# Kernel optimization log

Hardware: AMD Instinct MI355X
Metric: run time of the kernel (lower is better)

The kernel has to match this reference:

```python
import jax, jax.numpy as jnp
import numpy as np

B, P, F = 8, 8192, 32          # clouds, points per cloud, feature dim
RATIO, R, K = 0.25, 0.2, 64    # fps ratio, ball radius, max neighbors
M = int(P * RATIO)             # centroids per cloud


def setup_inputs() -> dict:
    key = jax.random.key(0)
    ks = jax.random.split(key, 6)
    pos = jax.random.uniform(ks[0], (B * P, 3), dtype=jnp.float32)
    batch = jnp.repeat(jnp.arange(B, dtype=jnp.int32), P)
    x = jax.random.normal(ks[1], (B * P, F), dtype=jnp.float32)

    def lin(k, i, o):
        return jax.random.normal(k, (i, o), dtype=jnp.float32) * (1.0 / np.sqrt(i))

    return {
        "pos": pos, "batch": batch, "x": x,
        "W1": lin(ks[2], F + 3, 64), "b1": jnp.zeros((64,), jnp.float32),
        "W2": lin(ks[3], 64, 64),    "b2": jnp.zeros((64,), jnp.float32),
        "W3": lin(ks[4], 64, 128),   "b3": jnp.zeros((128,), jnp.float32),
    }


def _fps(pos_b):
    """Farthest point sampling on one cloud [P,3] -> [M] indices (start at 0)."""
    d0 = jnp.full((P,), jnp.inf, pos_b.dtype)

    def step(carry, _):
        dists, last = carry
        d = jnp.sum((pos_b - pos_b[last]) ** 2, axis=-1)
        dists = jnp.minimum(dists, d)
        nxt = jnp.argmax(dists).astype(jnp.int32)
        return (dists, nxt), nxt

    _, idx = jax.lax.scan(step, (d0, jnp.int32(0)), None, length=M - 1)
    return jnp.concatenate([jnp.zeros((1,), jnp.int32), idx])


def reference(pos, batch, x, W1, b1, W2, b2, W3, b3):
    posb = pos.reshape(B, P, 3)
    xb = x.reshape(B, P, F)

    # --- FPS: pick M pivot points per cloud ---
    idx = jax.vmap(_fps)(posb)                                   # [B,M]
    cent = jnp.take_along_axis(posb, idx[..., None], axis=1)     # [B,M,3]

    # --- radius ball query: up to K neighbors within R (lowest indices first) ---
    d2 = jnp.sum((cent[:, :, None, :] - posb[:, None, :, :]) ** 2, axis=-1)  # [B,M,P]
    in_ball = d2 <= R * R
    nb = jnp.sort(jnp.where(in_ball, jnp.arange(P)[None, None, :], P), axis=-1)[..., :K]
    valid = nb < P                                               # [B,M,K]
    nb_safe = jnp.where(valid, nb, 0)

    # --- gather -> point_filter MLP -> masked max aggregation (PointNetConv) ---
    pos_j = jax.vmap(lambda p, i: p[i])(posb, nb_safe)           # [B,M,K,3]
    x_j = jax.vmap(lambda f, i: f[i])(xb, nb_safe)               # [B,M,K,F]
    msg = jnp.concatenate([x_j, pos_j - cent[:, :, None, :]], axis=-1)  # [B,M,K,F+3]
    h = jax.nn.relu(msg @ W1 + b1)
    h = jax.nn.relu(h @ W2 + b2)
    h = jax.nn.relu(h @ W3 + b3)                                 # [B,M,K,128]
    neg = jnp.finfo(h.dtype).min
    h = jnp.where(valid[..., None], h, neg)
    out = jnp.max(h, axis=2)  # every centroid is its own neighbor -> non-empty

    centr_batch = jnp.repeat(jnp.arange(B, dtype=batch.dtype), M)
    return cent.reshape(B * M, 3), out.reshape(B * M, 128), centr_batch
```

## Files before the change

kernel.cpp:

```cpp
#include <hip/hip_runtime.h>
#include <stdint.h>
#include <math.h>

constexpr int kB = 8;
constexpr int kP = 8192;
constexpr int kF = 32;
constexpr int kM = 2048;
constexpr int kK = 64;
constexpr int kH = 64;
constexpr int kO = 128;

typedef float v2f __attribute__((ext_vector_type(2)));

__device__ __forceinline__ float dist2(float ax, float ay, float az,
                                       float bx, float by, float bz) {
#pragma clang fp contract(off)
    float dx = ax - bx, dy = ay - by, dz = az - bz;
    return (dx * dx + dy * dy) + dz * dz;
}

template <int CTRL>
__device__ __forceinline__ void dpp_max_step(unsigned int& khi, unsigned int& klo) {
    unsigned int ohi = (unsigned int)__builtin_amdgcn_update_dpp(
        0, (int)khi, CTRL, 0xf, 0xf, true);
    unsigned int olo = (unsigned int)__builtin_amdgcn_update_dpp(
        0, (int)klo, CTRL, 0xf, 0xf, true);
    bool take = (ohi > khi) || (ohi == khi && olo > klo);
    khi = take ? ohi : khi;
    klo = take ? olo : klo;
}

__global__ void init_kernel(int* __restrict__ prog) {
    if (threadIdx.x < 128) prog[threadIdx.x] = 0;
}

union SharedU {
    struct {
        float sxp[kP], syp[kP], szp[kP];
        unsigned short widx[kM];
        unsigned long long part[2][4];
    } f;
    struct {
        float msg[kK][36];
        float h1[kK][kH];
        float h2[kK][kH];
        float red[2][kO];
        int   s_nb[kK];
        float s_cent[3];
        int   s_cnt;
    } c;
};

__global__ __launch_bounds__(256, 1) void mega_kernel(
    const float* __restrict__ pos, const float* __restrict__ x,
    const float* __restrict__ W1, const float* __restrict__ b1,
    const float* __restrict__ W2, const float* __restrict__ b2,
    const float* __restrict__ W3, const float* __restrict__ b3,
    unsigned int* __restrict__ stage, int* __restrict__ prog,
    float* __restrict__ cent_out, float* __restrict__ feat_out,
    float* __restrict__ batch_out) {
    __shared__ SharedU sh;

    const int tid = threadIdx.x;
    const int wave = tid >> 6, lane = tid & 63;

    if (blockIdx.x < (unsigned)kB) {
        const int b = blockIdx.x;
        const float* pb = pos + (size_t)b * kP * 3;

        v2f px2[16], py2[16], pz2[16], dd2[16];
#pragma unroll
        for (int q = 0; q < 32; ++q) {
            int i = tid + q * 256;
            float X = pb[i * 3 + 0];
            float Y = pb[i * 3 + 1];
            float Z = pb[i * 3 + 2];
            sh.f.sxp[i] = X; sh.f.syp[i] = Y; sh.f.szp[i] = Z;
            if (q & 1) { px2[q >> 1].y = X; py2[q >> 1].y = Y; pz2[q >> 1].y = Z; }
            else       { px2[q >> 1].x = X; py2[q >> 1].x = Y; pz2[q >> 1].x = Z; }
        }
#pragma unroll
        for (int q = 0; q < 16; ++q) dd2[q] = (v2f){INFINITY, INFINITY};

        if (tid == 0) sh.f.widx[0] = 0;
        __syncthreads();

        float lx = sh.f.sxp[0], ly = sh.f.syp[0], lz = sh.f.szp[0];
        if (tid == 0) {
            size_t o = (size_t)(b * kM) * 3;
            __hip_atomic_store(&stage[o + 0], __float_as_uint(lx),
                               __ATOMIC_RELAXED, __HIP_MEMORY_SCOPE_AGENT);
            __hip_atomic_store(&stage[o + 1], __float_as_uint(ly),
                               __ATOMIC_RELAXED, __HIP_MEMORY_SCOPE_AGENT);
            __hip_atomic_store(&stage[o + 2], __float_as_uint(lz),
                               __ATOMIC_RELAXED, __HIP_MEMORY_SCOPE_AGENT);
            __hip_atomic_store(&prog[b * 16], 1,
                               __ATOMIC_RELEASE, __HIP_MEMORY_SCOPE_AGENT);
        }

        for (int m = 1; m < kM; ++m) {
            v2f lxv = {lx, lx}, lyv = {ly, ly}, lzv = {lz, lz};
#pragma unroll
            for (int q = 0; q < 16; ++q) {
#pragma clang fp contract(off)
                v2f dx = px2[q] - lxv;
                v2f dy = py2[q] - lyv;
                v2f dz = pz2[q] - lzv;
                v2f d2 = (dx * dx + dy * dy) + dz * dz;
                dd2[q].x = fminf(dd2[q].x, d2.x);
                dd2[q].y = fminf(dd2[q].y, d2.y);
            }

            v2f t0 = {fmaxf(dd2[0].x, dd2[0].y), fmaxf(dd2[1].x, dd2[1].y)};
            v2f t1 = {fmaxf(dd2[2].x, dd2[2].y), fmaxf(dd2[3].x, dd2[3].y)};
            v2f t2 = {fmaxf(dd2[4].x, dd2[4].y), fmaxf(dd2[5].x, dd2[5].y)};
            v2f t3 = {fmaxf(dd2[6].x, dd2[6].y), fmaxf(dd2[7].x, dd2[7].y)};
            v2f t4 = {fmaxf(dd2[8].x, dd2[8].y), fmaxf(dd2[9].x, dd2[9].y)};
            v2f t5 = {fmaxf(dd2[10].x, dd2[10].y), fmaxf(dd2[11].x, dd2[11].y)};
            v2f t6 = {fmaxf(dd2[12].x, dd2[12].y), fmaxf(dd2[13].x, dd2[13].y)};
            v2f t7 = {fmaxf(dd2[14].x, dd2[14].y), fmaxf(dd2[15].x, dd2[15].y)};
            float u0 = fmaxf(fmaxf(t0.x, t0.y), fmaxf(t1.x, t1.y));
            float u1 = fmaxf(fmaxf(t2.x, t2.y), fmaxf(t3.x, t3.y));
            float u2 = fmaxf(fmaxf(t4.x, t4.y), fmaxf(t5.x, t5.y));
            float u3 = fmaxf(fmaxf(t6.x, t6.y), fmaxf(t7.x, t7.y));
            float bv = fmaxf(fmaxf(u0, u1), fmaxf(u2, u3));

            int lqs[4];
#pragma unroll
            for (int g = 0; g < 4; ++g) {
                int t = 64;
#pragma unroll
                for (int s = 7; s >= 0; --s) {
                    int sl = g * 8 + s;
                    float v = (sl & 1) ? dd2[sl >> 1].y : dd2[sl >> 1].x;
                    t = (v == bv) ? sl : t;
                }
                lqs[g] = t;
            }
            int bq = lqs[3];
            bq = (lqs[2] < 64) ? lqs[2] : bq;
            bq = (lqs[1] < 64) ? lqs[1] : bq;
            bq = (lqs[0] < 64) ? lqs[0] : bq;

            unsigned int bidx = (unsigned int)(tid + bq * 256);
            unsigned int khi = __float_as_uint(bv);
            unsigned int klo = (unsigned int)(~bidx);

            dpp_max_step<0x111>(khi, klo);
            dpp_max_step<0x112>(khi, klo);
            dpp_max_step<0x114>(khi, klo);
            dpp_max_step<0x118>(khi, klo);
            dpp_max_step<0x142>(khi, klo);
            dpp_max_step<0x143>(khi, klo);
            if (lane == 63)
                sh.f.part[m & 1][wave] = ((unsigned long long)khi << 32) | klo;
            __syncthreads();

            unsigned long long k = sh.f.part[m & 1][0];
#pragma unroll
            for (int w = 1; w < 4; ++w) {
                unsigned long long o = sh.f.part[m & 1][w];
                if (o > k) k = o;
            }
            unsigned int wi = ~(unsigned int)k;
            lx = sh.f.sxp[wi]; ly = sh.f.syp[wi]; lz = sh.f.szp[wi];
            if (tid == 0) sh.f.widx[m] = (unsigned short)wi;

            if ((m & 31) == 31) {
                int m0 = m - 31;
                if (tid < 96) {
                    int mm = m0 + tid / 3;
                    int comp = tid % 3;
                    unsigned int w2 = (mm == m) ? wi
                                                : (unsigned int)sh.f.widx[mm];
                    float v = (comp == 0) ? sh.f.sxp[w2]
                            : (comp == 1) ? sh.f.syp[w2] : sh.f.szp[w2];
                    __hip_atomic_store(&stage[(size_t)(b * kM + mm) * 3 + comp],
                                       __float_as_uint(v),
                                       __ATOMIC_RELAXED, __HIP_MEMORY_SCOPE_AGENT);
                }
                __syncthreads();
                if (tid == 0)
                    __hip_atomic_store(&prog[b * 16], m + 1,
                                       __ATOMIC_RELEASE, __HIP_MEMORY_SCOPE_AGENT);
            }
        }
        __syncthreads();

#pragma unroll
        for (int q = 0; q < kM / 256; ++q) {
            int i = tid + q * 256;
            unsigned int wi = sh.f.widx[i];
            size_t o = (size_t)(b * kM + i) * 3;
            cent_out[o + 0] = sh.f.sxp[wi];
            cent_out[o + 1] = sh.f.syp[wi];
            cent_out[o + 2] = sh.f.szp[wi];
        }
        return;
    }

    const int i = (int)blockIdx.x - kB;
    const int b = i & 7;
    const int cl = i >> 3;
    const int c = b * kM + cl;

    if (tid == 0) {
        int p;
        while ((p = __hip_atomic_load(&prog[b * 16], __ATOMIC_ACQUIRE,
                                      __HIP_MEMORY_SCOPE_AGENT)) < cl + 1) {
            if (cl + 1 - p > 128) __builtin_amdgcn_s_sleep(64);
            else                  __builtin_amdgcn_s_sleep(8);
        }
    }
    __syncthreads();

    if (tid < 3) {
        unsigned int u = __hip_atomic_load(&stage[(size_t)c * 3 + tid],
                                           __ATOMIC_RELAXED, __HIP_MEMORY_SCOPE_AGENT);
        sh.c.s_cent[tid] = __uint_as_float(u);
    }
    __syncthreads();

    if (wave == 0) {
        const float R2 = (float)(0.2 * 0.2);
        float cx = sh.c.s_cent[0], cy = sh.c.s_cent[1], cz = sh.c.s_cent[2];
        const float* pb = pos + (size_t)b * kP * 3;
        int cnt = 0;
        for (int p0 = 0; p0 < kP && cnt < kK; p0 += 64) {
            int idx = p0 + lane;
            float X = pb[idx * 3 + 0], Y = pb[idx * 3 + 1], Z = pb[idx * 3 + 2];
            float d2 = dist2(X, Y, Z, cx, cy, cz);
            bool in = d2 <= R2;
            unsigned long long mask = __ballot(in);
            int rank = __popcll(mask & ((1ull << lane) - 1ull));
            if (in && cnt + rank < kK) sh.c.s_nb[cnt + rank] = idx;
            cnt = min(cnt + (int)__popcll(mask), kK);
        }
        if (lane == 0) { sh.c.s_cnt = cnt; batch_out[c] = (float)b; }
    }
    __syncthreads();
    const int cnt = sh.c.s_cnt;

    for (int u = tid; u < kK * 35; u += 256) {
        int k = u / 35, f = u - k * 35;
        float v = 0.0f;
        if (k < cnt) {
            int n = sh.c.s_nb[k];
            if (f < 32) v = x[((size_t)b * kP + n) * kF + f];
            else        v = pos[((size_t)b * kP + n) * 3 + (f - 32)] - sh.c.s_cent[f - 32];
        }
        sh.c.msg[k][f] = v;
    }
    __syncthreads();

    {
        int j = tid & 63, k0 = tid >> 6;
        float w[35];
#pragma unroll
        for (int q = 0; q < 35; ++q) w[q] = W1[q * 64 + j];
        float bb = b1[j];
#pragma unroll
        for (int kk = 0; kk < 16; ++kk) {
            int k = k0 * 16 + kk;
            float acc = bb;
#pragma unroll
            for (int q = 0; q < 35; ++q) acc += sh.c.msg[k][q] * w[q];
            sh.c.h1[k][j] = fmaxf(acc, 0.0f);
        }
    }
    __syncthreads();

    {
        int j = tid & 63, k0 = tid >> 6;
        float w[64];
#pragma unroll
        for (int q = 0; q < 64; ++q) w[q] = W2[q * 64 + j];
        float bb = b2[j];
#pragma unroll
        for (int kk = 0; kk < 16; ++kk) {
            int k = k0 * 16 + kk;
            float acc = bb;
#pragma unroll
            for (int q = 0; q < 64; ++q) acc += sh.c.h1[k][q] * w[q];
            sh.c.h2[k][j] = fmaxf(acc, 0.0f);
        }
    }
    __syncthreads();

    {
        int j = tid & 127, k0 = tid >> 7;
        float w[64];
#pragma unroll
        for (int q = 0; q < 64; ++q) w[q] = W3[q * 128 + j];
        float bb = b3[j];
        float best = -INFINITY;
        for (int kk = 0; kk < 32; ++kk) {
            int k = k0 * 32 + kk;
            if (k >= cnt) break;
            float acc = bb;
#pragma unroll
            for (int q = 0; q < 64; ++q) acc += sh.c.h2[k][q] * w[q];
            best = fmaxf(best, fmaxf(acc, 0.0f));
        }
        sh.c.red[k0][j] = best;
    }
    __syncthreads();

    if (tid < kO) {
        float o = fmaxf(sh.c.red[0][tid], sh.c.red[1][tid]);
        feat_out[(size_t)c * kO + tid] = o;
    }
}

extern "C" void kernel_launch(void* const* d_in, const int* in_sizes, int n_in,
                              void* d_out, int out_size, void* d_ws, size_t ws_size,
                              hipStream_t stream) {
    const float* pos = (const float*)d_in[0];
    const float* x  = (const float*)d_in[2];
    const float* W1 = (const float*)d_in[3];
    const float* b1 = (const float*)d_in[4];
    const float* W2 = (const float*)d_in[5];
    const float* b2 = (const float*)d_in[6];
    const float* W3 = (const float*)d_in[7];
    const float* b3 = (const float*)d_in[8];

    float* out = (float*)d_out;
    float* cent_out  = out;
    float* feat_out  = out + (size_t)kB * kM * 3;
    float* batch_out = out + (size_t)kB * kM * (3 + kO);

    char* ws = (char*)d_ws;
    int* prog           = (int*)ws;
    unsigned int* stage = (unsigned int*)(ws + 512);

    init_kernel<<<1, 128, 0, stream>>>(prog);
    mega_kernel<<<kB + kB * kM, 256, 0, stream>>>(
        pos, x, W1, b1, W2, b2, W3, b3, stage, prog,
        cent_out, feat_out, batch_out);
}
```

Before: 2.492 ms.

## Process four centroids per block and run the MLP on fp16 MFMA

Each consumer block now handles four centroids, one per wave. Each wave runs its own ball query and gathers its neighbors straight into fp16 shared tiles. The three MLP layers are rewritten as 16x16x32 f16 MFMA tiles against transposed fp16 weights staged once per block, with the masked max taken from the accumulators. This removes scalar FP32 FMA loops and cuts the block count fourfold, which spreads weight-loading cost across more work. The price is reduced fp16 precision for activations and weights, and each block must wait for four centroids from FPS before it starts.

```diff
diff --git a/kernel.cpp b/kernel.cpp
--- a/kernel.cpp
+++ b/kernel.cpp
@@ -7,10 +7,11 @@
 constexpr int kF = 32;
 constexpr int kM = 2048;
 constexpr int kK = 64;
-constexpr int kH = 64;
 constexpr int kO = 128;
 
 typedef float v2f __attribute__((ext_vector_type(2)));
+typedef _Float16 h8 __attribute__((ext_vector_type(8)));
+typedef float f4v __attribute__((ext_vector_type(4)));
 
 __device__ __forceinline__ float dist2(float ax, float ay, float az,
                                        float bx, float by, float bz) {
@@ -41,13 +42,15 @@
         unsigned long long part[2][4];
     } f;
     struct {
-        float msg[kK][36];
-        float h1[kK][kH];
-        float h2[kK][kH];
-        float red[2][kO];
-        int   s_nb[kK];
-        float s_cent[3];
-        int   s_cnt;
+        _Float16 A0[256][72];
+        _Float16 A1[256][72];
+        _Float16 Wt1[64][72];
+        _Float16 Wt2[64][72];
+        _Float16 Wt3[128][72];
+        float bias[256];
+        float red[4][4][128];
+        int   s_nb[4][kK];
+        int   s_cnt[4];
     } c;
 };
 
@@ -201,29 +204,39 @@
 
     const int i = (int)blockIdx.x - kB;
     const int b = i & 7;
-    const int cl = i >> 3;
-    const int c = b * kM + cl;
+    const int cl0 = (i >> 3) * 4;
+
+    for (int idx = tid; idx < 64 * 64; idx += 256) {
+        int n = idx & 63, kk = idx >> 6;
+        sh.c.Wt1[n][kk] = (_Float16)((kk < 35) ? W1[kk * 64 + n] : 0.0f);
+        sh.c.Wt2[n][kk] = (_Float16)W2[kk * 64 + n];
+    }
+    for (int idx = tid; idx < 64 * 128; idx += 256) {
+        int n = idx & 127, kk = idx >> 7;
+        sh.c.Wt3[n][kk] = (_Float16)W3[kk * 128 + n];
+    }
+    sh.c.bias[tid] = (tid < 64) ? b1[tid] : (tid < 128) ? b2[tid - 64]
+                                                        : b3[tid - 128];
 
     if (tid == 0) {
         int p;
         while ((p = __hip_atomic_load(&prog[b * 16], __ATOMIC_ACQUIRE,
-                                      __HIP_MEMORY_SCOPE_AGENT)) < cl + 1) {
-            if (cl + 1 - p > 128) __builtin_amdgcn_s_sleep(64);
-            else                  __builtin_amdgcn_s_sleep(8);
-        }
-    }
-    __syncthreads();
-
-    if (tid < 3) {
-        unsigned int u = __hip_atomic_load(&stage[(size_t)c * 3 + tid],
-                                           __ATOMIC_RELAXED, __HIP_MEMORY_SCOPE_AGENT);
-        sh.c.s_cent[tid] = __uint_as_float(u);
-    }
-    __syncthreads();
-
-    if (wave == 0) {
+                                      __HIP_MEMORY_SCOPE_AGENT)) < cl0 + 4) {
+            if (cl0 + 4 - p > 128) __builtin_amdgcn_s_sleep(64);
+            else                   __builtin_amdgcn_s_sleep(8);
+        }
+    }
+    __syncthreads();
+
+    const int c = b * kM + cl0 + wave;
+    float cx = __uint_as_float(__hip_atomic_load(&stage[(size_t)c * 3 + 0],
+                   __ATOMIC_RELAXED, __HIP_MEMORY_SCOPE_AGENT));
+    float cy = __uint_as_float(__hip_atomic_load(&stage[(size_t)c * 3 + 1],
+                   __ATOMIC_RELAXED, __HIP_MEMORY_SCOPE_AGENT));
+    float cz = __uint_as_float(__hip_atomic_load(&stage[(size_t)c * 3 + 2],
+                   __ATOMIC_RELAXED, __HIP_MEMORY_SCOPE_AGENT));
+    {
         const float R2 = (float)(0.2 * 0.2);
-        float cx = sh.c.s_cent[0], cy = sh.c.s_cent[1], cz = sh.c.s_cent[2];
         const float* pb = pos + (size_t)b * kP * 3;
         int cnt = 0;
         for (int p0 = 0; p0 < kP && cnt < kK; p0 += 64) {
@@ -233,82 +246,149 @@
             bool in = d2 <= R2;
             unsigned long long mask = __ballot(in);
             int rank = __popcll(mask & ((1ull << lane) - 1ull));
-            if (in && cnt + rank < kK) sh.c.s_nb[cnt + rank] = idx;
+            if (in && cnt + rank < kK) sh.c.s_nb[wave][cnt + rank] = idx;
             cnt = min(cnt + (int)__popcll(mask), kK);
         }
-        if (lane == 0) { sh.c.s_cnt = cnt; batch_out[c] = (float)b; }
-    }
-    __syncthreads();
-    const int cnt = sh.c.s_cnt;
-
-    for (int u = tid; u < kK * 35; u += 256) {
-        int k = u / 35, f = u - k * 35;
-        float v = 0.0f;
-        if (k < cnt) {
-            int n = sh.c.s_nb[k];
-            if (f < 32) v = x[((size_t)b * kP + n) * kF + f];
-            else        v = pos[((size_t)b * kP + n) * 3 + (f - 32)] - sh.c.s_cent[f - 32];
-        }
-        sh.c.msg[k][f] = v;
-    }
-    __syncthreads();
-
-    {
-        int j = tid & 63, k0 = tid >> 6;
-        float w[35];
-#pragma unroll
-        for (int q = 0; q < 35; ++q) w[q] = W1[q * 64 + j];
-        float bb = b1[j];
-#pragma unroll
-        for (int kk = 0; kk < 16; ++kk) {
-            int k = k0 * 16 + kk;
-            float acc = bb;
-#pragma unroll
-            for (int q = 0; q < 35; ++q) acc += sh.c.msg[k][q] * w[q];
-            sh.c.h1[k][j] = fmaxf(acc, 0.0f);
-        }
-    }
-    __syncthreads();
-
-    {
-        int j = tid & 63, k0 = tid >> 6;
-        float w[64];
-#pragma unroll
-        for (int q = 0; q < 64; ++q) w[q] = W2[q * 64 + j];
-        float bb = b2[j];
-#pragma unroll
-        for (int kk = 0; kk < 16; ++kk) {
-            int k = k0 * 16 + kk;
-            float acc = bb;
-#pragma unroll
-            for (int q = 0; q < 64; ++q) acc += sh.c.h1[k][q] * w[q];
-            sh.c.h2[k][j] = fmaxf(acc, 0.0f);
-        }
-    }
-    __syncthreads();
-
-    {
-        int j = tid & 127, k0 = tid >> 7;
-        float w[64];
-#pragma unroll
-        for (int q = 0; q < 64; ++q) w[q] = W3[q * 128 + j];
-        float bb = b3[j];
-        float best = -INFINITY;
-        for (int kk = 0; kk < 32; ++kk) {
-            int k = k0 * 32 + kk;
-            if (k >= cnt) break;
-            float acc = bb;
-#pragma unroll
-            for (int q = 0; q < 64; ++q) acc += sh.c.h2[k][q] * w[q];
-            best = fmaxf(best, fmaxf(acc, 0.0f));
-        }
-        sh.c.red[k0][j] = best;
-    }
-    __syncthreads();
-
-    if (tid < kO) {
-        float o = fmaxf(sh.c.red[0][tid], sh.c.red[1][tid]);
-        feat_out[(size_t)c * kO + tid] = o;
+        if (lane == 0) { sh.c.s_cnt[wave] = cnt; batch_out[c] = (float)b; }
+    }
+    __syncthreads();
+    const int cntw = sh.c.s_cnt[wave];
+
+    {
+        int k = lane;
+        if (k < cntw) {
+            int n = sh.c.s_nb[wave][k];
+            const float4* xr4 = (const float4*)(x + ((size_t)b * kP + n) * kF);
+#pragma unroll
+            for (int t = 0; t < 4; ++t) {
+                float4 a4 = xr4[2 * t], c4 = xr4[2 * t + 1];
+                h8 o = {(_Float16)a4.x, (_Float16)a4.y, (_Float16)a4.z,
+                        (_Float16)a4.w, (_Float16)c4.x, (_Float16)c4.y,
+                        (_Float16)c4.z, (_Float16)c4.w};
+                *(h8*)&sh.c.A0[tid][t * 8] = o;
+            }
+            float dx = pos[((size_t)b * kP + n) * 3 + 0] - cx;
+            float dy = pos[((size_t)b * kP + n) * 3 + 1] - cy;
+            float dz = pos[((size_t)b * kP + n) * 3 + 2] - cz;
+            h8 o4 = {(_Float16)dx, (_Float16)dy, (_Float16)dz,
+                     (_Float16)0.f, (_Float16)0.f, (_Float16)0.f,
+                     (_Float16)0.f, (_Float16)0.f};
+            *(h8*)&sh.c.A0[tid][32] = o4;
+            h8 z = {};
+            *(h8*)&sh.c.A0[tid][40] = z;
+            *(h8*)&sh.c.A0[tid][48] = z;
+            *(h8*)&sh.c.A0[tid][56] = z;
+        } else {
+            h8 z = {};
+#pragma unroll
+            for (int t = 0; t < 8; ++t) *(h8*)&sh.c.A0[tid][t * 8] = z;
+        }
+    }
+    __syncthreads();
+
+    const int m16 = lane & 15, quad = lane >> 4;
+
+    {
+        h8 bf[4][2];
+#pragma unroll
+        for (int nt = 0; nt < 4; ++nt)
+#pragma unroll
+            for (int kc = 0; kc < 2; ++kc)
+                bf[nt][kc] = *(const h8*)&sh.c.Wt1[nt * 16 + m16][kc * 32 + quad * 8];
+#pragma unroll
+        for (int mt = 0; mt < 4; ++mt) {
+            int m0 = wave * 64 + mt * 16;
+            h8 a0 = *(const h8*)&sh.c.A0[m0 + m16][quad * 8];
+            h8 a1 = *(const h8*)&sh.c.A0[m0 + m16][32 + quad * 8];
+#pragma unroll
+            for (int nt = 0; nt < 4; ++nt) {
+                f4v acc = {0.f, 0.f, 0.f, 0.f};
+                acc = __builtin_amdgcn_mfma_f32_16x16x32_f16(a0, bf[nt][0], acc, 0, 0, 0);
+                acc = __builtin_amdgcn_mfma_f32_16x16x32_f16(a1, bf[nt][1], acc, 0, 0, 0);
+                int n = nt * 16 + m16;
+                float bb = sh.c.bias[n];
+#pragma unroll
+                for (int r = 0; r < 4; ++r)
+                    sh.c.A1[m0 + quad * 4 + r][n] =
+                        (_Float16)fmaxf(acc[r] + bb, 0.0f);
+            }
+        }
+    }
+    __syncthreads();
+
+    {
+        h8 bf[4][2];
+#pragma unroll
+        for (int nt = 0; nt < 4; ++nt)
+#pragma unroll
+            for (int kc = 0; kc < 2; ++kc)
+                bf[nt][kc] = *(const h8*)&sh.c.Wt2[nt * 16 + m16][kc * 32 + quad * 8];
+#pragma unroll
+        for (int mt = 0; mt < 4; ++mt) {
+            int m0 = wave * 64 + mt * 16;
+            h8 a0 = *(const h8*)&sh.c.A1[m0 + m16][quad * 8];
+            h8 a1 = *(const h8*)&sh.c.A1[m0 + m16][32 + quad * 8];
+#pragma unroll
+            for (int nt = 0; nt < 4; ++nt) {
+                f4v acc = {0.f, 0.f, 0.f, 0.f};
+                acc = __builtin_amdgcn_mfma_f32_16x16x32_f16(a0, bf[nt][0], acc, 0, 0, 0);
+                acc = __builtin_amdgcn_mfma_f32_16x16x32_f16(a1, bf[nt][1], acc, 0, 0, 0);
+                int n = nt * 16 + m16;
+                float bb = sh.c.bias[64 + n];
+#pragma unroll
+                for (int r = 0; r < 4; ++r)
+                    sh.c.A0[m0 + quad * 4 + r][n] =
+                        (_Float16)fmaxf(acc[r] + bb, 0.0f);
+            }
+        }
+    }
+    __syncthreads();
+
+    {
+        h8 bf[8][2];
+#pragma unroll
+        for (int nt = 0; nt < 8; ++nt)
+#pragma unroll
+            for (int kc = 0; kc < 2; ++kc)
+                bf[nt][kc] = *(const h8*)&sh.c.Wt3[nt * 16 + m16][kc * 32 + quad * 8];
+        float best[8];
+#pragma unroll
+        for (int nt = 0; nt < 8; ++nt) best[nt] = -INFINITY;
+#pragma unroll
+        for (int mt = 0; mt < 4; ++mt) {
+            int m0 = wave * 64 + mt * 16;
+            h8 a0 = *(const h8*)&sh.c.A0[m0 + m16][quad * 8];
+            h8 a1 = *(const h8*)&sh.c.A0[m0 + m16][32 + quad * 8];
+#pragma unroll
+            for (int nt = 0; nt < 8; ++nt) {
+                f4v acc = {0.f, 0.f, 0.f, 0.f};
+                acc = __builtin_amdgcn_mfma_f32_16x16x32_f16(a0, bf[nt][0], acc, 0, 0, 0);
+                acc = __builtin_amdgcn_mfma_f32_16x16x32_f16(a1, bf[nt][1], acc, 0, 0, 0);
+                int n = nt * 16 + m16;
+                float bb = sh.c.bias[128 + n];
+#pragma unroll
+                for (int r = 0; r < 4; ++r) {
+                    int krow = mt * 16 + quad * 4 + r;
+                    float v = fmaxf(acc[r] + bb, 0.0f);
+                    if (krow < cntw) best[nt] = fmaxf(best[nt], v);
+                }
+            }
+        }
+#pragma unroll
+        for (int nt = 0; nt < 8; ++nt)
+            sh.c.red[wave][quad][nt * 16 + m16] = best[nt];
+    }
+    __syncthreads();
+
+    {
+        int w2 = tid >> 6, n = tid & 63;
+#pragma unroll
+        for (int h = 0; h < 2; ++h) {
+            int n2 = n + h * 64;
+            float o = fmaxf(fmaxf(sh.c.red[w2][0][n2], sh.c.red[w2][1][n2]),
+                            fmaxf(sh.c.red[w2][2][n2], sh.c.red[w2][3][n2]));
+            feat_out[(size_t)(b * kM + cl0 + w2) * kO + n2] = o;
+        }
     }
 }
 
@@ -334,7 +414,7 @@
     unsigned int* stage = (unsigned int*)(ws + 512);
 
     init_kernel<<<1, 128, 0, stream>>>(prog);
-    mega_kernel<<<kB + kB * kM, 256, 0, stream>>>(
+    mega_kernel<<<kB + (kB * kM) / 4, 256, 0, stream>>>(
         pos, x, W1, b1, W2, b2, W3, b3, stage, prog,
         cent_out, feat_out, batch_out);
 }
```

Measured after the change: 2.153 ms (median of 2 runs). 1.16x faster.
